# Kernel tuning notes

Hardware: AMD Instinct MI355X
Metric: run time of the kernel (lower is better)

## Reference

```python
import jax, jax.numpy as jnp
import numpy as np

B, N, S, F = 16384, 1152, 576, 8  # batch, n_sites, n_symm, features
LOG2 = float(np.log(2.0))


def log_cosh(x):
    # numerically stable log(cosh(x)) = |x| + log1p(exp(-2|x|)) - log(2)
    a = jnp.abs(x)
    return a + jnp.log1p(jnp.exp(-2.0 * a)) - LOG2


def setup_inputs() -> dict:
    key = jax.random.key(0)
    ks = iter(jax.random.split(key, 32))
    f32 = jnp.float32
    d = {}
    d['x'] = jax.random.normal(next(ks), (B, N), dtype=f32)
    d['symmetries'] = jax.random.randint(next(ks), (S, N), 0, N, dtype=jnp.int32)
    d['corr0'] = jax.random.randint(next(ks), (576, 4), 0, N, dtype=jnp.int32)
    d['corr1'] = jax.random.randint(next(ks), (576, 4), 0, N, dtype=jnp.int32)
    d['corr2'] = jax.random.randint(next(ks), (24, 24), 0, N, dtype=jnp.int32)
    d['corr3'] = jax.random.randint(next(ks), (24, 24), 0, N, dtype=jnp.int32)
    d['corr0_symm'] = jax.random.randint(next(ks), (S, 576), 0, 576, dtype=jnp.int32)
    d['corr1_symm'] = jax.random.randint(next(ks), (S, 576), 0, 576, dtype=jnp.int32)
    d['corr2_symm'] = jax.random.randint(next(ks), (S, 24), 0, 24, dtype=jnp.int32)
    d['corr3_symm'] = jax.random.randint(next(ks), (S, 24), 0, 24, dtype=jnp.int32)
    std = 0.01
    d['hidden_bias'] = std * jax.random.normal(next(ks), (F,), dtype=f32)
    d['symm_kernel'] = std * jax.random.normal(next(ks), (F, N), dtype=f32)
    d['visible_bias'] = std * jax.random.normal(next(ks), (2,), dtype=f32)
    d['corr0_bias'] = std * jax.random.normal(next(ks), (1,), dtype=f32)
    d['corr0_kernel'] = std * jax.random.normal(next(ks), (F, 576), dtype=f32)
    d['corr1_bias'] = std * jax.random.normal(next(ks), (1,), dtype=f32)
    d['corr1_kernel'] = std * jax.random.normal(next(ks), (F, 576), dtype=f32)
    d['corr2_bias'] = std * jax.random.normal(next(ks), (1,), dtype=f32)
    d['corr2_kernel'] = std * jax.random.normal(next(ks), (F, 24), dtype=f32)
    d['corr3_bias'] = std * jax.random.normal(next(ks), (1,), dtype=f32)
    d['corr3_kernel'] = std * jax.random.normal(next(ks), (F, 24), dtype=f32)
    d['loop0_hidden_bias'] = std * jax.random.normal(next(ks), (F,), dtype=f32)
    d['loop0_kernel'] = std * jax.random.normal(next(ks), (F, 24), dtype=f32)
    d['loop1_hidden_bias'] = std * jax.random.normal(next(ks), (F,), dtype=f32)
    d['loop1_kernel'] = std * jax.random.normal(next(ks), (F, 24), dtype=f32)
    return d


def reference(x, symmetries, corr0, corr1, corr2, corr3,
              corr0_symm, corr1_symm, corr2_symm, corr3_symm,
              hidden_bias, symm_kernel, visible_bias,
              corr0_bias, corr0_kernel, corr1_bias, corr1_kernel,
              corr2_bias, corr2_kernel, corr3_bias, corr3_kernel,
              loop0_hidden_bias, loop0_kernel, loop1_hidden_bias, loop1_kernel):
    n_batch = x.shape[0]
    # symmetrized kernel: (F, S, N)
    K = jnp.take(symm_kernel, symmetries, axis=1)
    theta = jnp.einsum('bn,fsn->bfs', x, K)  # (B, F, S)
    theta = theta + hidden_bias[:, None]
    bias = jnp.sum(x.reshape(n_batch, -1, 2), axis=1) @ visible_bias  # (B,)

    correlators = [corr0, corr1, corr2, corr3]
    corr_symms = [corr0_symm, corr1_symm, corr2_symm, corr3_symm]
    corr_biases = [corr0_bias, corr1_bias, corr2_bias, corr3_bias]
    corr_kernels = [corr0_kernel, corr1_kernel, corr2_kernel, corr3_kernel]

    corr_values = []
    for corr, csym, cb, ck in zip(correlators, corr_symms, corr_biases, corr_kernels):
        ckk = jnp.take(ck, csym, axis=1)               # (F, S, C)
        cv = jnp.take(x, corr, axis=1).prod(axis=2)    # (B, C)
        corr_values.append(cv)
        theta = theta + jnp.einsum('bc,fsc->bfs', cv, ckk)
        bias = bias + cb * jnp.sum(cv, axis=1)

    out = jnp.sum(log_cosh(theta), axis=(1, 2))  # (B,)

    # last two correlators are loop correlators with dedicated hidden units
    loop_params = [(loop0_hidden_bias, loop0_kernel, corr2_symm, corr_values[2]),
                   (loop1_hidden_bias, loop1_kernel, corr3_symm, corr_values[3])]
    for lhb, lk, lsym, lv in loop_params:
        lkk = jnp.take(lk, lsym, axis=1)                      # (F, S, C)
        lt = jnp.einsum('bc,fsc->bfs', lv, lkk) + lhb[:, None]
        out = out + jnp.sum(log_cosh(lt), axis=(1, 2))

    return out + bias
```

## Files before the change

kernel.cpp:

```cpp
#include <hip/hip_runtime.h>
#include <math.h>

#define B_    16384
#define N_    1152
#define KPAD  2496
#define NK    39
#define KLOOP 256
#define NOUT  4608
#define NT2   18
#define LOG2F_ 0.69314718055994530942f

typedef unsigned short ushort_t;
typedef __attribute__((ext_vector_type(8))) short short8;
typedef __attribute__((ext_vector_type(4))) float floatx4;

__device__ __forceinline__ float log_cosh_f(float t) {
    float a = fabsf(t);
    return a + __logf(1.0f + __expf(-2.0f * a)) - LOG2F_;
}
__device__ __forceinline__ ushort_t bf16_rne(float f) {
    unsigned int u = __float_as_uint(f);
    return (ushort_t)((u + 0x7fffu + ((u >> 16) & 1u)) >> 16);
}
__device__ __forceinline__ float bf16_to_f(ushort_t h) {
    return __uint_as_float(((unsigned int)h) << 16);
}

typedef __attribute__((address_space(1))) const unsigned int guint;
typedef __attribute__((address_space(3))) unsigned int luint;
__device__ __forceinline__ void gload16(const ushort_t* src, ushort_t* dst) {
    __builtin_amdgcn_global_load_lds((guint*)src, (luint*)dst, 16, 0, 0);
}

__global__ __launch_bounds__(256) void build_w(
    const int* __restrict__ symm,
    const int* __restrict__ c0s, const int* __restrict__ c1s,
    const int* __restrict__ c2s, const int* __restrict__ c3s,
    const float* __restrict__ sk,
    const float* __restrict__ ck0, const float* __restrict__ ck1,
    const float* __restrict__ ck2, const float* __restrict__ ck3,
    const float* __restrict__ l0k, const float* __restrict__ l1k,
    ushort_t* __restrict__ Wb, ushort_t* __restrict__ LWb)
{
    __shared__ int idx[2352];
    const int s = blockIdx.x;
    const int tid = threadIdx.x;
    for (int i = tid; i < 1152; i += 256) idx[i] = symm[s * N_ + i];
    for (int i = tid; i < 576; i += 256) idx[1152 + i] = c0s[s * 576 + i];
    for (int i = tid; i < 576; i += 256) idx[1728 + i] = c1s[s * 576 + i];
    if (tid < 24) idx[2304 + tid] = c2s[s * 24 + tid];
    else if (tid < 48) idx[2328 + (tid - 24)] = c3s[s * 24 + (tid - 24)];
    __syncthreads();
    for (int f = 0; f < 8; ++f) {
        ushort_t* wr = Wb + (size_t)(s * 8 + f) * KPAD;
        for (int k = tid; k < KPAD; k += 256) {
            ushort_t o;
            if (k < 1152)      o = bf16_rne(sk[f * N_ + idx[k]]);
            else if (k < 1728) o = bf16_rne(ck0[f * 576 + idx[k]]);
            else if (k < 2304) o = bf16_rne(ck1[f * 576 + idx[k]]);
            else if (k < 2448) {
                int q = k - 2304, g = q / 48, c = q - g * 48;
                float w = (c < 24) ? ck2[f * 24 + idx[2304 + c]]
                                   : ck3[f * 24 + idx[2328 + (c - 24)]];
                ushort_t hi = bf16_rne(w);
                o = (g < 2) ? hi : bf16_rne(w - bf16_to_f(hi));
            } else o = 0;
            wr[k] = o;
        }
        ushort_t* lr = LWb + (size_t)(s * 8 + f) * KLOOP;
        for (int k2 = tid; k2 < KLOOP; k2 += 256) {
            int j2 = k2 >> 7, q = k2 & 127;
            ushort_t o = 0;
            if (q < 72) {
                int g = q / 24, c = q - g * 24;
                float w = j2 ? l1k[f * 24 + idx[2328 + c]]
                             : l0k[f * 24 + idx[2304 + c]];
                ushort_t hi = bf16_rne(w);
                o = (g < 2) ? hi : bf16_rne(w - bf16_to_f(hi));
            }
            lr[k2] = o;
        }
    }
}

__global__ __launch_bounds__(256) void build_cv(
    const float* __restrict__ x,
    const int* __restrict__ corr0, const int* __restrict__ corr1,
    const int* __restrict__ corr2, const int* __restrict__ corr3,
    const float* __restrict__ vb,
    const float* __restrict__ cb0, const float* __restrict__ cb1,
    const float* __restrict__ cb2, const float* __restrict__ cb3,
    ushort_t* __restrict__ XA, ushort_t* __restrict__ CVL,
    float* __restrict__ initb)
{
    __shared__ float xs[N_];
    __shared__ float red[256];
    __shared__ float cvhi[48], cvlo[48];
    const int tid = threadIdx.x;
    const int b = blockIdx.x;
    ushort_t* xr = XA + (size_t)b * KPAD;

    float bias = 0.f;
    const float vb0 = vb[0], vb1 = vb[1];
    for (int i = tid; i < N_; i += 256) {
        float v = x[(size_t)b * N_ + i];
        xs[i] = v;
        bias += v * ((i & 1) ? vb1 : vb0);
        xr[i] = bf16_rne(v);
    }
    __syncthreads();
    float s0 = 0.f, s1 = 0.f, s2 = 0.f, s3 = 0.f;
    for (int c = tid; c < 576; c += 256) {
        const int* i0 = corr0 + c * 4;
        float p = xs[i0[0]] * xs[i0[1]] * xs[i0[2]] * xs[i0[3]];
        xr[1152 + c] = bf16_rne(p); s0 += p;
        const int* i1 = corr1 + c * 4;
        float q = xs[i1[0]] * xs[i1[1]] * xs[i1[2]] * xs[i1[3]];
        xr[1728 + c] = bf16_rne(q); s1 += q;
    }
    if (tid < 48) {
        int j2 = tid / 24, c = tid - j2 * 24;
        const int* ii = (j2 ? corr3 : corr2) + c * 24;
        float p = 1.f;
        for (int j = 0; j < 24; ++j) p *= xs[ii[j]];
        float hv = bf16_to_f(bf16_rne(p));
        cvhi[tid] = hv;
        cvlo[tid] = p - hv;
        if (j2) s3 = p; else s2 = p;
    }
    __syncthreads();
    for (int i = tid; i < 192; i += 256) {
        ushort_t o = 0;
        if (i < 144) {
            int g = i / 48, c = i - g * 48;
            o = bf16_rne(g == 1 ? cvlo[c] : cvhi[c]);
        }
        xr[2304 + i] = o;
    }
    ushort_t* cr = CVL + (size_t)b * KLOOP;
    for (int k2 = tid; k2 < KLOOP; k2 += 256) {
        int j2 = k2 >> 7, q = k2 & 127;
        ushort_t o = 0;
        if (q < 72) {
            int g = q / 24, c = q - g * 24;
            o = bf16_rne(g == 1 ? cvlo[j2 * 24 + c] : cvhi[j2 * 24 + c]);
        }
        cr[k2] = o;
    }
    bias += cb0[0] * s0 + cb1[0] * s1 + cb2[0] * s2 + cb3[0] * s3;
    red[tid] = bias;
    __syncthreads();
    for (int off = 128; off; off >>= 1) {
        if (tid < off) red[tid] += red[tid + off];
        __syncthreads();
    }
    if (tid == 0) initb[b] = red[0];
}

__global__ __launch_bounds__(512, 2) void mfma_gemm(
    const ushort_t* __restrict__ XA, const ushort_t* __restrict__ Wb,
    const ushort_t* __restrict__ CVL, const ushort_t* __restrict__ LWb,
    const float* __restrict__ hidden_bias,
    const float* __restrict__ l0hb, const float* __restrict__ l1hb,
    float* __restrict__ partials)
{
    __shared__ __align__(16) ushort_t sh[65536];
    ushort_t* const A0 = sh;
    ushort_t* const B0 = sh + 16384;
    ushort_t* const A1 = sh + 32768;
    ushort_t* const B1 = sh + 49152;

    const int tid = threadIdx.x;
    const int l = tid & 63, w = tid >> 6;
    const int wm = w >> 2, wn = w & 3;
    const int lrow = l & 15, lg = l >> 4;
    const int lr8 = l >> 3;
    const int lsw = ((l & 7) ^ lr8) * 8;

    const int bid = blockIdx.x;
    const int swz = (bid & 7) * 144 + (bid >> 3);
    const int nt = swz % NT2, bt = swz / NT2;
    const int n0 = nt * 256, b0 = bt * 256;

    const ushort_t* XAb  = XA  + (size_t)b0 * KPAD;
    const ushort_t* Wbb  = Wb  + (size_t)n0 * KPAD;
    const ushort_t* CVb  = CVL + (size_t)b0 * KLOOP;
    const ushort_t* LWbb = LWb + (size_t)n0 * KLOOP;

    floatx4 acc[8][4];

    auto STAGE = [&](const ushort_t* Ag, int sA, const ushort_t* Bg, int sB,
                     int kg, ushort_t* Ab, ushort_t* Bb) {
#pragma unroll
        for (int i = 0; i < 4; ++i) {
            const int r0 = w * 32 + i * 8;
            gload16(Ag + (size_t)(r0 + lr8) * sA + kg + lsw, &Ab[r0 * 64]);
            gload16(Bg + (size_t)(r0 + lr8) * sB + kg + lsw, &Bb[r0 * 64]);
        }
    };
    auto COMPUTE = [&](const ushort_t* Ab, const ushort_t* Bb) {
#pragma unroll
        for (int ks = 0; ks < 2; ++ks) {
            short8 af[8], bfr[4];
#pragma unroll
            for (int mi = 0; mi < 8; ++mi)
                af[mi] = *(const short8*)&Ab[(wm * 128 + mi * 16 + lrow) * 64 +
                                             (((ks << 2) + lg) ^ (lrow & 7)) * 8];
#pragma unroll
            for (int ni = 0; ni < 4; ++ni)
                bfr[ni] = *(const short8*)&Bb[(wn * 64 + ni * 16 + lrow) * 64 +
                                              (((ks << 2) + lg) ^ (lrow & 7)) * 8];
#pragma unroll
            for (int mi = 0; mi < 8; ++mi)
#pragma unroll
                for (int ni = 0; ni < 4; ++ni)
                    acc[mi][ni] = __builtin_amdgcn_mfma_f32_16x16x32_bf16(
                        af[mi], bfr[ni], acc[mi][ni], 0, 0, 0);
        }
    };

#pragma unroll
    for (int mi = 0; mi < 8; ++mi)
#pragma unroll
        for (int ni = 0; ni < 4; ++ni) acc[mi][ni] = (floatx4){0.f, 0.f, 0.f, 0.f};

    STAGE(XAb, KPAD, Wbb, KPAD, 0, A0, B0);
    __syncthreads();
#pragma unroll 1
    for (int t = 0; t < NK; ++t) {
        ushort_t* Ac = (t & 1) ? A1 : A0;
        ushort_t* Bc = (t & 1) ? B1 : B0;
        if (t + 1 < NK)
            STAGE(XAb, KPAD, Wbb, KPAD, (t + 1) * 64,
                  (t & 1) ? A0 : A1, (t & 1) ? B0 : B1);
        COMPUTE(Ac, Bc);
        __syncthreads();
    }

    float rs[32];
    {
        const float hbv = hidden_bias[l & 7];
#pragma unroll
        for (int mi = 0; mi < 8; ++mi)
#pragma unroll
            for (int reg = 0; reg < 4; ++reg) {
                float t = 0.f;
#pragma unroll
                for (int ni = 0; ni < 4; ++ni)
                    t += log_cosh_f(acc[mi][ni][reg] + hbv);
                rs[mi * 4 + reg] = t;
            }
    }

#pragma unroll 1
    for (int j2 = 0; j2 < 2; ++j2) {
#pragma unroll
        for (int mi = 0; mi < 8; ++mi)
#pragma unroll
            for (int ni = 0; ni < 4; ++ni) acc[mi][ni] = (floatx4){0.f, 0.f, 0.f, 0.f};
        STAGE(CVb, KLOOP, LWbb, KLOOP, j2 * 128, A0, B0);
        __syncthreads();
        STAGE(CVb, KLOOP, LWbb, KLOOP, j2 * 128 + 64, A1, B1);
        COMPUTE(A0, B0);
        __syncthreads();
        COMPUTE(A1, B1);
        const float lbv = (j2 ? l1hb : l0hb)[l & 7];
#pragma unroll
        for (int mi = 0; mi < 8; ++mi)
#pragma unroll
            for (int reg = 0; reg < 4; ++reg) {
                float t = 0.f;
#pragma unroll
                for (int ni = 0; ni < 4; ++ni)
                    t += log_cosh_f(acc[mi][ni][reg] + lbv);
                rs[mi * 4 + reg] += t;
            }
    }

    __syncthreads();
    float* red = (float*)sh;
#pragma unroll
    for (int mi = 0; mi < 8; ++mi)
#pragma unroll
        for (int reg = 0; reg < 4; ++reg) {
            float v = rs[mi * 4 + reg];
            v += __shfl_xor(v, 1);
            v += __shfl_xor(v, 2);
            v += __shfl_xor(v, 4);
            v += __shfl_xor(v, 8);
            if (lrow == 0)
                red[(wm * 128 + mi * 16 + lg * 4 + reg) * 5 + wn] = v;
        }
    __syncthreads();
    if (tid < 256) {
        float t = red[tid * 5 + 0] + red[tid * 5 + 1] +
                  red[tid * 5 + 2] + red[tid * 5 + 3];
        partials[(size_t)nt * B_ + b0 + tid] = t;
    }
}

__global__ __launch_bounds__(256) void finalize_out(
    const float* __restrict__ initb, const float* __restrict__ partials,
    float* __restrict__ out)
{
    int b = blockIdx.x * 256 + threadIdx.x;
    float s = initb[b];
#pragma unroll
    for (int t = 0; t < NT2; ++t) s += partials[(size_t)t * B_ + b];
    out[b] = s;
}

extern "C" void kernel_launch(void* const* d_in, const int* in_sizes, int n_in,
                              void* d_out, int out_size, void* d_ws, size_t ws_size,
                              hipStream_t stream) {
    const float* x    = (const float*)d_in[0];
    const int* symm   = (const int*)d_in[1];
    const int* corr0  = (const int*)d_in[2];
    const int* corr1  = (const int*)d_in[3];
    const int* corr2  = (const int*)d_in[4];
    const int* corr3  = (const int*)d_in[5];
    const int* c0s    = (const int*)d_in[6];
    const int* c1s    = (const int*)d_in[7];
    const int* c2s    = (const int*)d_in[8];
    const int* c3s    = (const int*)d_in[9];
    const float* hb   = (const float*)d_in[10];
    const float* sk   = (const float*)d_in[11];
    const float* vb   = (const float*)d_in[12];
    const float* cb0  = (const float*)d_in[13];
    const float* ck0  = (const float*)d_in[14];
    const float* cb1  = (const float*)d_in[15];
    const float* ck1  = (const float*)d_in[16];
    const float* cb2  = (const float*)d_in[17];
    const float* ck2  = (const float*)d_in[18];
    const float* cb3  = (const float*)d_in[19];
    const float* ck3  = (const float*)d_in[20];
    const float* l0hb = (const float*)d_in[21];
    const float* l0k  = (const float*)d_in[22];
    const float* l1hb = (const float*)d_in[23];
    const float* l1k  = (const float*)d_in[24];

    ushort_t* wsu = (ushort_t*)d_ws;
    ushort_t* Wb  = wsu;
    ushort_t* XA  = Wb + (size_t)NOUT * KPAD;
    ushort_t* LWb = XA + (size_t)B_ * KPAD;
    ushort_t* CVL = LWb + (size_t)NOUT * KLOOP;
    float* initb    = (float*)(CVL + (size_t)B_ * KLOOP);
    float* partials = initb + B_;

    build_w<<<576, 256, 0, stream>>>(
        symm, c0s, c1s, c2s, c3s, sk, ck0, ck1, ck2, ck3, l0k, l1k, Wb, LWb);
    build_cv<<<B_, 256, 0, stream>>>(
        x, corr0, corr1, corr2, corr3, vb, cb0, cb1, cb2, cb3, XA, CVL, initb);
    mfma_gemm<<<1152, 512, 0, stream>>>(
        XA, Wb, CVL, LWb, hb, l0hb, l1hb, partials);
    finalize_out<<<B_ / 256, 256, 0, stream>>>(initb, partials, (float*)d_out);
}
```

Measured before the change: 650.2 us.

## Rework main GEMM into 4-stage K=32 LDS pipeline with vmcnt waits

Measured after the change: 621.4 us. 1.05x faster.

```diff
diff --git a/kernel.cpp b/kernel.cpp
--- a/kernel.cpp
+++ b/kernel.cpp
@@ -3,8 +3,8 @@
 
 #define B_    16384
 #define N_    1152
-#define KPAD  2496
-#define NK    39
+#define KPAD  2560
+#define NK32  80
 #define KLOOP 256
 #define NOUT  4608
 #define NT2   18
@@ -31,6 +31,11 @@
 __device__ __forceinline__ void gload16(const ushort_t* src, ushort_t* dst) {
     __builtin_amdgcn_global_load_lds((guint*)src, (luint*)dst, 16, 0, 0);
 }
+
+#define PIPE_WAIT(N) do {                                     \
+    asm volatile("s_waitcnt vmcnt(" #N ")" ::: "memory");     \
+    __builtin_amdgcn_s_barrier();                             \
+    asm volatile("" ::: "memory"); } while (0)
 
 __global__ __launch_bounds__(256) void build_w(
     const int* __restrict__ symm,
@@ -129,7 +134,7 @@
         if (j2) s3 = p; else s2 = p;
     }
     __syncthreads();
-    for (int i = tid; i < 192; i += 256) {
+    for (int i = tid; i < KPAD - 2304; i += 256) {
         ushort_t o = 0;
         if (i < 144) {
             int g = i / 48, c = i - g * 48;
@@ -165,17 +170,17 @@
     float* __restrict__ partials)
 {
     __shared__ __align__(16) ushort_t sh[65536];
-    ushort_t* const A0 = sh;
-    ushort_t* const B0 = sh + 16384;
-    ushort_t* const A1 = sh + 32768;
-    ushort_t* const B1 = sh + 49152;
+    ushort_t* const A0 = sh;                 ushort_t* const Bu0 = sh + 8192;
+    ushort_t* const A1 = sh + 16384;         ushort_t* const Bu1 = sh + 24576;
+    ushort_t* const A2 = sh + 32768;         ushort_t* const Bu2 = sh + 40960;
+    ushort_t* const A3 = sh + 49152;         ushort_t* const Bu3 = sh + 57344;
 
     const int tid = threadIdx.x;
     const int l = tid & 63, w = tid >> 6;
     const int wm = w >> 2, wn = w & 3;
     const int lrow = l & 15, lg = l >> 4;
-    const int lr8 = l >> 3;
-    const int lsw = ((l & 7) ^ lr8) * 8;
+    const int srow = l >> 2;
+    const int sgr8 = ((l & 3) ^ (srow & 3)) * 8;
 
     const int bid = blockIdx.x;
     const int swz = (bid & 7) * 144 + (bid >> 3);
@@ -189,34 +194,49 @@
 
     floatx4 acc[8][4];
 
-    auto STAGE = [&](const ushort_t* Ag, int sA, const ushort_t* Bg, int sB,
-                     int kg, ushort_t* Ab, ushort_t* Bb) {
-#pragma unroll
-        for (int i = 0; i < 4; ++i) {
-            const int r0 = w * 32 + i * 8;
-            gload16(Ag + (size_t)(r0 + lr8) * sA + kg + lsw, &Ab[r0 * 64]);
-            gload16(Bg + (size_t)(r0 + lr8) * sB + kg + lsw, &Bb[r0 * 64]);
+    auto STG = [&](const ushort_t* g, int stride, int kg, ushort_t* lbase) {
+#pragma unroll
+        for (int i = 0; i < 2; ++i) {
+            const int r0 = i * 128 + w * 16;
+            gload16(g + (size_t)(r0 + srow) * stride + kg + sgr8,
+                    lbase + r0 * 32);
         }
     };
-    auto COMPUTE = [&](const ushort_t* Ab, const ushort_t* Bb) {
-#pragma unroll
-        for (int ks = 0; ks < 2; ++ks) {
-            short8 af[8], bfr[4];
-#pragma unroll
-            for (int mi = 0; mi < 8; ++mi)
-                af[mi] = *(const short8*)&Ab[(wm * 128 + mi * 16 + lrow) * 64 +
-                                             (((ks << 2) + lg) ^ (lrow & 7)) * 8];
+
+    const int ga = (lg ^ (lrow & 3)) * 8;
+    const int abase = (wm * 128 + lrow) * 32 + ga;
+    const int bbase = (wn * 64 + lrow) * 32 + ga;
+
+    auto TILE = [&](const ushort_t* Ab, const ushort_t* Bb,
+                    int kgn, ushort_t* An, ushort_t* Bn, bool doStage) {
+        short8 af[4], af2[4], bfr[4];
+#pragma unroll
+        for (int mi = 0; mi < 4; ++mi)
+            af[mi] = *(const short8*)(Ab + abase + mi * 512);
+#pragma unroll
+        for (int ni = 0; ni < 4; ++ni)
+            bfr[ni] = *(const short8*)(Bb + bbase + ni * 512);
+        if (doStage) { STG(XAb, KPAD, kgn, An); STG(Wbb, KPAD, kgn, Bn); }
+        asm volatile("" ::: "memory");
+        __builtin_amdgcn_s_setprio(1);
+#pragma unroll
+        for (int mi = 0; mi < 4; ++mi)
 #pragma unroll
             for (int ni = 0; ni < 4; ++ni)
-                bfr[ni] = *(const short8*)&Bb[(wn * 64 + ni * 16 + lrow) * 64 +
-                                              (((ks << 2) + lg) ^ (lrow & 7)) * 8];
-#pragma unroll
-            for (int mi = 0; mi < 8; ++mi)
-#pragma unroll
-                for (int ni = 0; ni < 4; ++ni)
-                    acc[mi][ni] = __builtin_amdgcn_mfma_f32_16x16x32_bf16(
-                        af[mi], bfr[ni], acc[mi][ni], 0, 0, 0);
-        }
+                acc[mi][ni] = __builtin_amdgcn_mfma_f32_16x16x32_bf16(
+                    af[mi], bfr[ni], acc[mi][ni], 0, 0, 0);
+        __builtin_amdgcn_s_setprio(0);
+#pragma unroll
+        for (int mi = 0; mi < 4; ++mi)
+            af2[mi] = *(const short8*)(Ab + abase + 2048 + mi * 512);
+        __builtin_amdgcn_s_setprio(1);
+#pragma unroll
+        for (int mi = 0; mi < 4; ++mi)
+#pragma unroll
+            for (int ni = 0; ni < 4; ++ni)
+                acc[mi + 4][ni] = __builtin_amdgcn_mfma_f32_16x16x32_bf16(
+                    af2[mi], bfr[ni], acc[mi + 4][ni], 0, 0, 0);
+        __builtin_amdgcn_s_setprio(0);
     };
 
 #pragma unroll
@@ -224,18 +244,21 @@
 #pragma unroll
         for (int ni = 0; ni < 4; ++ni) acc[mi][ni] = (floatx4){0.f, 0.f, 0.f, 0.f};
 
-    STAGE(XAb, KPAD, Wbb, KPAD, 0, A0, B0);
-    __syncthreads();
+    STG(XAb, KPAD, 0, A0);  STG(Wbb, KPAD, 0, Bu0);
+    STG(XAb, KPAD, 32, A1); STG(Wbb, KPAD, 32, Bu1);
+    STG(XAb, KPAD, 64, A2); STG(Wbb, KPAD, 64, Bu2);
 #pragma unroll 1
-    for (int t = 0; t < NK; ++t) {
-        ushort_t* Ac = (t & 1) ? A1 : A0;
-        ushort_t* Bc = (t & 1) ? B1 : B0;
-        if (t + 1 < NK)
-            STAGE(XAb, KPAD, Wbb, KPAD, (t + 1) * 64,
-                  (t & 1) ? A0 : A1, (t & 1) ? B0 : B1);
-        COMPUTE(Ac, Bc);
-        __syncthreads();
-    }
+    for (int tt = 0; tt < 19; ++tt) {
+        const int t = tt * 4;
+        PIPE_WAIT(8); TILE(A0, Bu0, (t + 3) * 32, A3, Bu3, true);
+        PIPE_WAIT(8); TILE(A1, Bu1, (t + 4) * 32, A0, Bu0, true);
+        PIPE_WAIT(8); TILE(A2, Bu2, (t + 5) * 32, A1, Bu1, true);
+        PIPE_WAIT(8); TILE(A3, Bu3, (t + 6) * 32, A2, Bu2, true);
+    }
+    PIPE_WAIT(8); TILE(A0, Bu0, 79 * 32, A3, Bu3, true);
+    PIPE_WAIT(8); TILE(A1, Bu1, 0, A0, Bu0, false);
+    PIPE_WAIT(4); TILE(A2, Bu2, 0, A0, Bu0, false);
+    PIPE_WAIT(0); TILE(A3, Bu3, 0, A0, Bu0, false);
 
     float rs[32];
     {
@@ -258,12 +281,16 @@
         for (int mi = 0; mi < 8; ++mi)
 #pragma unroll
             for (int ni = 0; ni < 4; ++ni) acc[mi][ni] = (floatx4){0.f, 0.f, 0.f, 0.f};
-        STAGE(CVb, KLOOP, LWbb, KLOOP, j2 * 128, A0, B0);
         __syncthreads();
-        STAGE(CVb, KLOOP, LWbb, KLOOP, j2 * 128 + 64, A1, B1);
-        COMPUTE(A0, B0);
+        STG(CVb, KLOOP, j2 * 128 +  0, A0); STG(LWbb, KLOOP, j2 * 128 +  0, Bu0);
+        STG(CVb, KLOOP, j2 * 128 + 32, A1); STG(LWbb, KLOOP, j2 * 128 + 32, Bu1);
+        STG(CVb, KLOOP, j2 * 128 + 64, A2); STG(LWbb, KLOOP, j2 * 128 + 64, Bu2);
+        STG(CVb, KLOOP, j2 * 128 + 96, A3); STG(LWbb, KLOOP, j2 * 128 + 96, Bu3);
         __syncthreads();
-        COMPUTE(A1, B1);
+        TILE(A0, Bu0, 0, A0, Bu0, false);
+        TILE(A1, Bu1, 0, A0, Bu0, false);
+        TILE(A2, Bu2, 0, A0, Bu0, false);
+        TILE(A3, Bu3, 0, A0, Bu0, false);
         const float lbv = (j2 ? l1hb : l0hb)[l & 7];
 #pragma unroll
         for (int mi = 0; mi < 8; ++mi)
```
